# Kernel tuning notes

Measured on AMD Instinct MI355X. Metric: run time of the kernel, lower is better.

Reference implementation:

```python
import jax, jax.numpy as jnp
import numpy as np


def setup_inputs() -> dict:
    key = jax.random.key(0)
    ks = jax.random.split(key, 8)
    C = 512
    Cq = C // 8  # 64
    x = jax.random.normal(ks[0], (4, C, 64, 64), dtype=jnp.float32)
    # 1x1 conv == per-pixel linear; store weights as [out, in]
    Wq = jax.random.normal(ks[1], (Cq, C), dtype=jnp.float32) * (1.0 / np.sqrt(C))
    bq = jax.random.normal(ks[2], (Cq,), dtype=jnp.float32) * 0.01
    Wk = jax.random.normal(ks[3], (Cq, C), dtype=jnp.float32) * (1.0 / np.sqrt(C))
    bk = jax.random.normal(ks[4], (Cq,), dtype=jnp.float32) * 0.01
    Wv = jax.random.normal(ks[5], (C, C), dtype=jnp.float32) * (1.0 / np.sqrt(C))
    bv = jax.random.normal(ks[6], (C,), dtype=jnp.float32) * 0.01
    alpha = jax.random.normal(ks[7], (1,), dtype=jnp.float32)
    return {"x": x, "Wq": Wq, "bq": bq, "Wk": Wk, "bk": bk, "Wv": Wv, "bv": bv, "alpha": alpha}


def reference(x, Wq, bq, Wk, bk, Wv, bv, alpha):
    B, C, H, W = x.shape
    HW = H * W
    xf = x.reshape(B, C, HW)  # [B, C, HW]
    # 1x1 convs as channel matmuls
    q = jnp.einsum('oc,bcn->bon', Wq, xf) + bq[None, :, None]  # [B, Cq, HW]
    k = jnp.einsum('oc,bcn->bon', Wk, xf) + bk[None, :, None]  # [B, Cq, HW]
    v = jnp.einsum('oc,bcn->bon', Wv, xf) + bv[None, :, None]  # [B, C, HW]
    # attention[b, i, j] = softmax_j( q[:, i] . k[:, j] )
    scores = jnp.einsum('bci,bcj->bij', q, k)  # [B, HW, HW]
    attn = jax.nn.softmax(scores, axis=-1)
    # feat_e = v @ attn^T : out[b, c, i] = sum_j v[b, c, j] * attn[b, i, j]
    feat_e = jnp.einsum('bcj,bij->bci', v, attn).reshape(B, C, H, W)
    return alpha[0] * feat_e
```

## Files before the change

kernel.cpp:

```cpp
#include <hip/hip_runtime.h>
#include <hip/hip_fp16.h>

#define HW_N 4096
#define C_IN 512
#define C_Q  64
#define NB   4
#define M_Y  640
#define LOG2E 1.4426950408889634f

typedef __attribute__((ext_vector_type(8))) short short8;
typedef __attribute__((ext_vector_type(4))) short short4v;
typedef __attribute__((ext_vector_type(4))) float float4v;
typedef unsigned short ushort_t;

__device__ __forceinline__ ushort_t f2h(float x) {
    return __half_as_ushort(__float2half(x));
}
__device__ __forceinline__ float h2f(ushort_t h) {
    return __half2float(__ushort_as_half(h));
}
__device__ __forceinline__ void gl2lds16(const ushort_t* g, ushort_t* l) {
    __builtin_amdgcn_global_load_lds(
        (const __attribute__((address_space(1))) unsigned int*)g,
        (__attribute__((address_space(3))) unsigned int*)l, 16, 0, 0);
}

__global__ __launch_bounds__(256) void split_w(const float* __restrict__ Wq,
                                               const float* __restrict__ Wk,
                                               const float* __restrict__ Wv,
                                               ushort_t* __restrict__ Wh,
                                               ushort_t* __restrict__ Wl) {
    int idx = (blockIdx.x * 256 + threadIdx.x) * 4;
#pragma unroll
    for (int e = 0; e < 4; e++) {
        int i = idx + e;
        int m = i >> 9, k = i & 511;
        float v = (m < C_Q) ? Wq[m * C_IN + k]
                 : (m < 2 * C_Q) ? Wk[(m - C_Q) * C_IN + k]
                 : Wv[(size_t)(m - 2 * C_Q) * C_IN + k];
        ushort_t h = f2h(v);
        Wh[i] = h;
        Wl[i] = f2h(v - h2f(h));
    }
}

__global__ __launch_bounds__(256) void split_x(const float* __restrict__ x,
                                               ushort_t* __restrict__ xTh,
                                               ushort_t* __restrict__ xTl,
                                               float* __restrict__ D) {
    const size_t bz = blockIdx.z;
    x   += bz * ((size_t)C_IN * HW_N);
    xTh += bz * ((size_t)HW_N * C_IN);
    xTl += bz * ((size_t)HW_N * C_IN);
    D   += bz * HW_N;

    if (blockIdx.y == 0 && blockIdx.x < 16) D[blockIdx.x * 256 + threadIdx.x] = 0.f;

    __shared__ float tile[64][65];
    const int n0 = blockIdx.x * 64, k0 = blockIdx.y * 64;
    const int t = threadIdx.x;
#pragma unroll
    for (int it = 0; it < 4; it++) {
        int e = t + it * 256;
        int r = e >> 4, c4 = (e & 15) << 2;
        float4 v = *(const float4*)(x + (size_t)(k0 + r) * HW_N + n0 + c4);
        tile[r][c4 + 0] = v.x; tile[r][c4 + 1] = v.y;
        tile[r][c4 + 2] = v.z; tile[r][c4 + 3] = v.w;
    }
    __syncthreads();
    const int rr = t >> 2, kq = (t & 3) << 4;
    ushort_t h[16], l[16];
#pragma unroll
    for (int j = 0; j < 16; j++) {
        float v = tile[kq + j][rr];
        h[j] = f2h(v);
        l[j] = f2h(v - h2f(h[j]));
    }
    size_t o = (size_t)(n0 + rr) * C_IN + k0 + kq;
    *(uint4*)(xTh + o) = *(uint4*)h;
    *(uint4*)(xTh + o + 8) = *(uint4*)(h + 8);
    *(uint4*)(xTl + o) = *(uint4*)l;
    *(uint4*)(xTl + o + 8) = *(uint4*)(l + 8);
}

__global__ __launch_bounds__(256, 2) void ygemm(
    const ushort_t* __restrict__ Ah, const ushort_t* __restrict__ Al,
    const ushort_t* __restrict__ Bh, const ushort_t* __restrict__ Bl,
    const float* __restrict__ bq, const float* __restrict__ bk,
    const float* __restrict__ bv,
    ushort_t* __restrict__ qkTh, ushort_t* __restrict__ qkTl,
    ushort_t* __restrict__ Vh, ushort_t* __restrict__ Vl) {
    const size_t bz = blockIdx.z;
    Bh   += bz * ((size_t)HW_N * C_IN);
    Bl   += bz * ((size_t)HW_N * C_IN);
    qkTh += bz * ((size_t)HW_N * 2 * C_Q);
    qkTl += bz * ((size_t)HW_N * 2 * C_Q);
    Vh   += bz * ((size_t)C_IN * HW_N);
    Vl   += bz * ((size_t)C_IN * HW_N);

    __shared__ ushort_t sAh[2][128 * 32];
    __shared__ ushort_t sAl[2][128 * 32];
    __shared__ ushort_t sBh[2][128 * 32];
    __shared__ ushort_t sBl[2][128 * 32];

    const int tid = threadIdx.x, w = tid >> 6, lane = tid & 63;
    const int quad = lane >> 4, lr = lane & 15;
    const int m0 = blockIdx.y * 128, n0 = blockIdx.x * 128;

    const ushort_t* src;
    ushort_t* dst0;
    int rowBase;
    if (w == 0)      { src = Ah; dst0 = sAh[0]; rowBase = m0; }
    else if (w == 1) { src = Al; dst0 = sAl[0]; rowBase = m0; }
    else if (w == 2) { src = Bh; dst0 = sBh[0]; rowBase = n0; }
    else             { src = Bl; dst0 = sBl[0]; rowBase = n0; }
    const int cr = lane >> 2, uv = lane & 3;
    const int kcol = (uv ^ ((cr >> 1) & 3)) << 3;
    const ushort_t* gk = src + (size_t)(rowBase + cr) * C_IN + kcol;

    const int wm = (w & 1) * 64, wn = (w >> 1) * 64;
    const int up = (quad ^ ((lr >> 1) & 3)) << 3;

    float4v acc[4][4];
#pragma unroll
    for (int i = 0; i < 4; i++)
#pragma unroll
        for (int j = 0; j < 4; j++) acc[i][j] = (float4v){0.f, 0.f, 0.f, 0.f};

#pragma unroll
    for (int c = 0; c < 8; c++)
        gl2lds16(gk + (size_t)(c * 16) * C_IN, dst0 + c * 512);
    __syncthreads();

    const int NSTEP = C_IN / 32;
    for (int it = 0; it < NSTEP; ++it) {
        const int cur = it & 1, nxt = cur ^ 1;

        if (it + 1 < NSTEP) {
            ushort_t* db = dst0 + nxt * (128 * 32);
#pragma unroll
            for (int c = 0; c < 8; c++)
                gl2lds16(gk + (size_t)(c * 16) * C_IN + (it + 1) * 32, db + c * 512);
        }

        short8 ah[4], al[4], bh[4], bl[4];
#pragma unroll
        for (int i = 0; i < 4; i++) {
            ah[i] = *(const short8*)&sAh[cur][(wm + i * 16 + lr) * 32 + up];
            al[i] = *(const short8*)&sAl[cur][(wm + i * 16 + lr) * 32 + up];
            bh[i] = *(const short8*)&sBh[cur][(wn + i * 16 + lr) * 32 + up];
            bl[i] = *(const short8*)&sBl[cur][(wn + i * 16 + lr) * 32 + up];
        }
#pragma unroll
        for (int i = 0; i < 4; i++)
#pragma unroll
            for (int j = 0; j < 4; j++)
                acc[i][j] = __builtin_amdgcn_mfma_f32_16x16x32_f16(ah[i], bh[j], acc[i][j], 0, 0, 0);
#pragma unroll
        for (int i = 0; i < 4; i++)
#pragma unroll
            for (int j = 0; j < 4; j++)
                acc[i][j] = __builtin_amdgcn_mfma_f32_16x16x32_f16(ah[i], bl[j], acc[i][j], 0, 0, 0);
#pragma unroll
        for (int i = 0; i < 4; i++)
#pragma unroll
            for (int j = 0; j < 4; j++)
                acc[i][j] = __builtin_amdgcn_mfma_f32_16x16x32_f16(al[i], bh[j], acc[i][j], 0, 0, 0);
        __syncthreads();
    }

#pragma unroll
    for (int i = 0; i < 4; i++)
#pragma unroll
        for (int j = 0; j < 4; j++)
#pragma unroll
            for (int r = 0; r < 4; r++) {
                const int m = m0 + wm + i * 16 + quad * 4 + r;
                const int n = n0 + wn + j * 16 + lr;
                float bi = (m < C_Q) ? bq[m]
                          : (m < 2 * C_Q) ? bk[m - C_Q] : bv[m - 2 * C_Q];
                float v = acc[i][j][r] + bi;
                ushort_t h = f2h(v);
                ushort_t lo = f2h(v - h2f(h));
                if (m < 2 * C_Q) {
                    qkTh[(size_t)n * (2 * C_Q) + m] = h;
                    qkTl[(size_t)n * (2 * C_Q) + m] = lo;
                } else {
                    Vh[(size_t)(m - 2 * C_Q) * HW_N + n] = h;
                    Vl[(size_t)(m - 2 * C_Q) * HW_N + n] = lo;
                }
            }
}

__global__ __launch_bounds__(256, 2) void qkgemm(const ushort_t* __restrict__ qkTh_,
                                                 const ushort_t* __restrict__ qkTl_,
                                                 float* __restrict__ outF,
                                                 float* __restrict__ Dsum) {
    __shared__ ushort_t sAh[2][128 * 32];
    __shared__ ushort_t sAl[2][128 * 32];
    __shared__ ushort_t sBh[2][128 * 32];
    __shared__ ushort_t sBl[2][128 * 32];

    const int tid = threadIdx.x, w = tid >> 6, lane = tid & 63;
    const int quad = lane >> 4, lr = lane & 15;
    const int m0 = blockIdx.y * 128, n0 = blockIdx.x * 128;

    const ushort_t* src = ((w & 1) ? qkTl_ : qkTh_) + ((w >> 1) ? C_Q : 0);
    ushort_t* dst0 = (w == 0) ? sAh[0] : (w == 1) ? sAl[0]
                   : (w == 2) ? sBh[0] : sBl[0];
    const int rowBase = (w >> 1) ? n0 : m0;
    const int cr = lane >> 2, uv = lane & 3;
    const int kcol = (uv ^ ((cr >> 1) & 3)) << 3;
    const ushort_t* gk = src + (size_t)(rowBase + cr) * (2 * C_Q) + kcol;

    const int wm = (w & 1) * 64, wn = (w >> 1) * 64;
    const int up = (quad ^ ((lr >> 1) & 3)) << 3;

    float4v acc[4][4];
#pragma unroll
    for (int i = 0; i < 4; i++)
#pragma unroll
        for (int j = 0; j < 4; j++) acc[i][j] = (float4v){0.f, 0.f, 0.f, 0.f};

#pragma unroll
    for (int c = 0; c < 8; c++)
        gl2lds16(gk + (size_t)(c * 16) * (2 * C_Q), dst0 + c * 512);
    __syncthreads();

    const int NSTEP = C_Q / 32;
#pragma unroll
    for (int it = 0; it < NSTEP; ++it) {
        const int cur = it & 1, nxt = cur ^ 1;

        if (it + 1 < NSTEP) {
            ushort_t* db = dst0 + nxt * (128 * 32);
#pragma unroll
            for (int c = 0; c < 8; c++)
                gl2lds16(gk + (size_t)(c * 16) * (2 * C_Q) + (it + 1) * 32, db + c * 512);
        }

        short8 ah[4], al[4], bh[4], bl[4];
#pragma unroll
        for (int i = 0; i < 4; i++) {
            ah[i] = *(const short8*)&sAh[cur][(wm + i * 16 + lr) * 32 + up];
            al[i] = *(const short8*)&sAl[cur][(wm + i * 16 + lr) * 32 + up];
            bh[i] = *(const short8*)&sBh[cur][(wn + i * 16 + lr) * 32 + up];
            bl[i] = *(const short8*)&sBl[cur][(wn + i * 16 + lr) * 32 + up];
        }
#pragma unroll
        for (int i = 0; i < 4; i++)
#pragma unroll
            for (int j = 0; j < 4; j++)
                acc[i][j] = __builtin_amdgcn_mfma_f32_16x16x32_f16(ah[i], bh[j], acc[i][j], 0, 0, 0);
#pragma unroll
        for (int i = 0; i < 4; i++)
#pragma unroll
            for (int j = 0; j < 4; j++)
                acc[i][j] = __builtin_amdgcn_mfma_f32_16x16x32_f16(ah[i], bl[j], acc[i][j], 0, 0, 0);
#pragma unroll
        for (int i = 0; i < 4; i++)
#pragma unroll
            for (int j = 0; j < 4; j++)
                acc[i][j] = __builtin_amdgcn_mfma_f32_16x16x32_f16(al[i], bh[j], acc[i][j], 0, 0, 0);
        if (it + 1 < NSTEP) __syncthreads();
    }

#pragma unroll
    for (int i = 0; i < 4; i++) {
#pragma unroll
        for (int r = 0; r < 4; r++) {
            float s = 0.f;
#pragma unroll
            for (int j = 0; j < 4; j++) {
                const int m = m0 + wm + i * 16 + quad * 4 + r;
                const int n = n0 + wn + j * 16 + lr;
                outF[(size_t)m * HW_N + n] = acc[i][j][r];
                s += __expf(acc[i][j][r]);
            }
            s += __shfl_xor(s, 1);
            s += __shfl_xor(s, 2);
            s += __shfl_xor(s, 4);
            s += __shfl_xor(s, 8);
            if (lr == 0)
                atomicAdd(&Dsum[m0 + wm + i * 16 + quad * 4 + r], s);
        }
    }
}

__global__ __launch_bounds__(512, 2) void feat7(const ushort_t* __restrict__ Vh,
                                                const ushort_t* __restrict__ Vl,
                                                const float* __restrict__ S,
                                                const float* __restrict__ D,
                                                float* __restrict__ out,
                                                float* __restrict__ part,
                                                int kLen) {
    __shared__ ushort_t sVh[2][256 * 32];
    __shared__ ushort_t sVl[2][256 * 32];
    __shared__ ushort_t sP [2][256 * 32];

    const int tid = threadIdx.x, w = tid >> 6, lane = tid & 63;
    const int quad = lane >> 4, lr = lane & 15;
    const int m0 = blockIdx.y * 256, n0 = blockIdx.x * 256;
    const int k0 = blockIdx.z * kLen;

    const int crv = lane >> 2, uv = lane & 3;
    const int vcol = (uv ^ ((crv >> 1) & 3)) << 3;
    const ushort_t* vbase = (w < 4) ? Vh : Vl;
    const ushort_t* gVsrc[4];
    int sOfs[4];
#pragma unroll
    for (int c = 0; c < 4; c++) {
        const int chunk = ((w & 3) * 4 + c);
        gVsrc[c] = vbase + (size_t)(m0 + chunk * 16 + crv) * HW_N + vcol + k0;
        sOfs[c] = chunk * 512;
    }

    const int pr = tid >> 3, pu = tid & 7;
    const float* gS = S + (size_t)(n0 + pr) * HW_N + k0 + pu * 4;
    const int pdst = (((pu >> 1) ^ ((pr >> 1) & 3)) << 3) + ((pu & 1) << 2);
    float lrw[4];
#pragma unroll
    for (int c = 0; c < 4; c++) lrw[c] = -log2f(D[n0 + pr + 64 * c]);

    const int wm = (w & 3) * 64, wn = (w >> 2) * 128;

    float4 sreg[4];
    const int nIter = kLen >> 5;

    {
#pragma unroll
        for (int c = 0; c < 4; c++)
            sreg[c] = *(const float4*)(gS + (size_t)(64 * c) * HW_N);
#pragma unroll
        for (int c = 0; c < 4; c++) gl2lds16(gVsrc[c], ((w < 4) ? sVh : sVl)[0] + sOfs[c]);
#pragma unroll
        for (int c = 0; c < 4; c++) {
            ushort_t h4[4];
            h4[0] = f2h(exp2f(fmaf(sreg[c].x, LOG2E, lrw[c])));
            h4[1] = f2h(exp2f(fmaf(sreg[c].y, LOG2E, lrw[c])));
            h4[2] = f2h(exp2f(fmaf(sreg[c].z, LOG2E, lrw[c])));
            h4[3] = f2h(exp2f(fmaf(sreg[c].w, LOG2E, lrw[c])));
            *(short4v*)&sP[0][(pr + 64 * c) * 32 + pdst] = *(short4v*)h4;
        }
        if (nIter > 1) {
#pragma unroll
            for (int c = 0; c < 4; c++)
                sreg[c] = *(const float4*)(gS + (size_t)(64 * c) * HW_N + 32);
        }
    }
    __syncthreads();

    float4v acc[4][8];
#pragma unroll
    for (int i = 0; i < 4; i++)
#pragma unroll
        for (int j = 0; j < 8; j++) acc[i][j] = (float4v){0.f, 0.f, 0.f, 0.f};

    for (int it = 0; it < nIter; ++it) {
        const int kk = it << 5;
        const int cur = it & 1, nxt = cur ^ 1;

        if (it + 1 < nIter) {
            ushort_t* db = ((w < 4) ? sVh : sVl)[nxt];
#pragma unroll
            for (int c = 0; c < 4; c++) gl2lds16(gVsrc[c] + kk + 32, db + sOfs[c]);
        }

        short8 bh[8];
#pragma unroll
        for (int j = 0; j < 8; j++) {
            const int row = wn + j * 16 + lr;
            bh[j] = *(const short8*)&sP[cur][row * 32 + ((quad ^ ((lr >> 1) & 3)) << 3)];
        }

        if (it + 1 < nIter) {
#pragma unroll
            for (int c = 0; c < 4; c++) {
                ushort_t h4[4];
                h4[0] = f2h(exp2f(fmaf(sreg[c].x, LOG2E, lrw[c])));
                h4[1] = f2h(exp2f(fmaf(sreg[c].y, LOG2E, lrw[c])));
                h4[2] = f2h(exp2f(fmaf(sreg[c].z, LOG2E, lrw[c])));
                h4[3] = f2h(exp2f(fmaf(sreg[c].w, LOG2E, lrw[c])));
                *(short4v*)&sP[nxt][(pr + 64 * c) * 32 + pdst] = *(short4v*)h4;
            }
            if (it + 2 < nIter) {
#pragma unroll
                for (int c = 0; c < 4; c++)
                    sreg[c] = *(const float4*)(gS + (size_t)(64 * c) * HW_N + kk + 64);
            }
        }

#pragma unroll
        for (int i = 0; i < 4; i++) {
            const int row = wm + i * 16 + lr;
            const int up = (quad ^ ((lr >> 1) & 3)) << 3;
            short8 ah = *(const short8*)&sVh[cur][row * 32 + up];
            short8 al = *(const short8*)&sVl[cur][row * 32 + up];
#pragma unroll
            for (int j = 0; j < 8; j++)
                acc[i][j] = __builtin_amdgcn_mfma_f32_16x16x32_f16(ah, bh[j], acc[i][j], 0, 0, 0);
#pragma unroll
            for (int j = 0; j < 8; j++)
                acc[i][j] = __builtin_amdgcn_mfma_f32_16x16x32_f16(al, bh[j], acc[i][j], 0, 0, 0);
        }
        __syncthreads();
    }

    float* o = (blockIdx.z == 0) ? out
             : (part + (size_t)(blockIdx.z - 1) * ((size_t)C_IN * HW_N));
#pragma unroll
    for (int i = 0; i < 4; i++)
#pragma unroll
        for (int j = 0; j < 8; j++)
#pragma unroll
            for (int r = 0; r < 4; r++) {
                const int m = m0 + wm + i * 16 + quad * 4 + r;
                const int n = n0 + wn + j * 16 + lr;
                o[(size_t)m * HW_N + n] = acc[i][j][r];
            }
}

__global__ __launch_bounds__(256) void reduce_alphaN(float* __restrict__ out,
                                                     const float4* __restrict__ part,
                                                     size_t stride4,
                                                     const float* __restrict__ alpha,
                                                     int np) {
    const size_t i = (size_t)blockIdx.x * 256 + threadIdx.x;
    const float a = alpha[0];
    float4* out4 = (float4*)out;
    float4 s = out4[i];
    for (int p = 0; p < np; p++) {
        float4 t = part[i + (size_t)p * stride4];
        s.x += t.x; s.y += t.y; s.z += t.z; s.w += t.w;
    }
    float4 o;
    o.x = a * s.x; o.y = a * s.y; o.z = a * s.z; o.w = a * s.w;
    out4[i] = o;
}


extern "C" void kernel_launch(void* const* d_in, const int* in_sizes, int n_in,
                              void* d_out, int out_size, void* d_ws, size_t ws_size,
                              hipStream_t stream) {
    const float* x     = (const float*)d_in[0];
    const float* Wq    = (const float*)d_in[1];
    const float* bq    = (const float*)d_in[2];
    const float* Wk    = (const float*)d_in[3];
    const float* bk    = (const float*)d_in[4];
    const float* Wv    = (const float*)d_in[5];
    const float* bv    = (const float*)d_in[6];
    const float* alpha = (const float*)d_in[7];
    float* out = (float*)d_out;

    const size_t planeQK = (size_t)HW_N * 2 * C_Q;
    const size_t planeV  = (size_t)C_IN * HW_N;
    const size_t planeXT = (size_t)HW_N * C_IN;
    const size_t planeW  = (size_t)M_Y * C_IN;
    const size_t planeS  = (size_t)HW_N * HW_N;

    const size_t fusedBytes =
        (size_t)NB * HW_N * 4 + 2 * (size_t)NB * planeQK * 2 +
        2 * (size_t)NB * planeV * 2 + 2 * planeW * 2 + planeS * 4 +
        7 * planeV * 4;
    const bool fused = (ws_size >= fusedBytes);

    if (fused) {
        float* D4      = (float*)d_ws;
        ushort_t* qkTh4 = (ushort_t*)(D4 + (size_t)NB * HW_N);
        ushort_t* qkTl4 = qkTh4 + (size_t)NB * planeQK;
        ushort_t* Vh4   = qkTl4 + (size_t)NB * planeQK;
        ushort_t* Vl4   = Vh4 + (size_t)NB * planeV;
        ushort_t* Wh    = Vl4 + (size_t)NB * planeV;
        ushort_t* Wl    = Wh + planeW;
        float* scores   = (float*)(Wl + planeW);
        float* part     = scores + planeS;
        ushort_t* xTh4  = (ushort_t*)scores;
        ushort_t* xTl4  = xTh4 + (size_t)NB * planeXT;

        split_w<<<dim3(M_Y * C_IN / 4 / 256), dim3(256), 0, stream>>>(Wq, Wk, Wv, Wh, Wl);

        split_x<<<dim3(HW_N / 64, C_IN / 64, NB), dim3(256), 0, stream>>>(
            x, xTh4, xTl4, D4);
        ygemm<<<dim3(HW_N / 128, M_Y / 128, NB), dim3(256), 0, stream>>>(
            Wh, Wl, xTh4, xTl4, bq, bk, bv, qkTh4, qkTl4, Vh4, Vl4);

        for (int b = 0; b < NB; b++) {
            float* outb = out + (size_t)b * planeV;
            qkgemm<<<dim3(HW_N / 128, HW_N / 128), dim3(256), 0, stream>>>(
                qkTh4 + (size_t)b * planeQK, qkTl4 + (size_t)b * planeQK,
                scores, D4 + (size_t)b * HW_N);
            feat7<<<dim3(HW_N / 256, C_IN / 256, 8), dim3(512), 0, stream>>>(
                Vh4 + (size_t)b * planeV, Vl4 + (size_t)b * planeV,
                scores, D4 + (size_t)b * HW_N, outb, part, HW_N / 8);
            reduce_alphaN<<<dim3((C_IN * HW_N / 4) / 256), dim3(256), 0, stream>>>(
                outb, (const float4*)part, planeV / 4, alpha, 7);
        }
        return;
    }

    float* D = (float*)d_ws;
    ushort_t* qkTh = (ushort_t*)(D + HW_N);
    ushort_t* qkTl = qkTh + planeQK;
    ushort_t* Vh   = qkTl + planeQK;
    ushort_t* Vl   = Vh + planeV;
    ushort_t* Wh   = Vl + planeV;
    ushort_t* Wl   = Wh + planeW;
    float* scores  = (float*)(Wl + planeW);
    float* part    = scores + planeS;
    ushort_t* xTh  = (ushort_t*)scores;
    ushort_t* xTl  = xTh + planeXT;

    const size_t baseF = (size_t)(part - (float*)d_ws);
    const int zsplit = (ws_size >= (baseF + 7 * planeV) * sizeof(float)) ? 8 : 4;

    split_w<<<dim3(M_Y * C_IN / 4 / 256), dim3(256), 0, stream>>>(Wq, Wk, Wv, Wh, Wl);

    for (int b = 0; b < NB; b++) {
        const float* xb = x + (size_t)b * planeV;
        float* outb = out + (size_t)b * planeV;

        split_x<<<dim3(HW_N / 64, C_IN / 64, 1), dim3(256), 0, stream>>>(
            xb, xTh, xTl, D);
        ygemm<<<dim3(HW_N / 128, M_Y / 128, 1), dim3(256), 0, stream>>>(
            Wh, Wl, xTh, xTl, bq, bk, bv, qkTh, qkTl, Vh, Vl);
        qkgemm<<<dim3(HW_N / 128, HW_N / 128), dim3(256), 0, stream>>>(
            qkTh, qkTl, scores, D);
        feat7<<<dim3(HW_N / 256, C_IN / 256, zsplit), dim3(512), 0, stream>>>(
            Vh, Vl, scores, D, outb, part, HW_N / zsplit);
        reduce_alphaN<<<dim3((C_IN * HW_N / 4) / 256), dim3(256), 0, stream>>>(
            outb, (const float4*)part, planeV / 4, alpha, zsplit - 1);
    }
}
```

Before: 467.1 us.

## Enlarge ygemm tile to 256x256 with 512 threads and padded weight rows

Moves the projection GEMM from 128x128 tiles with 4 waves to 256x256 tiles with 8 waves, each wave computing a 64x128 sub-tile. The weight matrix is zero-padded from 640 to 768 rows so the M dimension divides by 256, and the rows past the real ones are skipped at store time. The goal is more operand reuse per LDS load and fewer blocks, which should cut global and LDS traffic per MFMA. The cost is about 20% wasted compute on padding rows, 128KB of LDS per block, a larger accumulator array with register pressure, and only 3x16x4 blocks in the grid.

```diff
diff --git a/kernel.cpp b/kernel.cpp
--- a/kernel.cpp
+++ b/kernel.cpp
@@ -6,6 +6,7 @@
 #define C_Q  64
 #define NB   4
 #define M_Y  640
+#define M_YP 768
 #define LOG2E 1.4426950408889634f
 
 typedef __attribute__((ext_vector_type(8))) short short8;
@@ -37,7 +38,8 @@
         int m = i >> 9, k = i & 511;
         float v = (m < C_Q) ? Wq[m * C_IN + k]
                  : (m < 2 * C_Q) ? Wk[(m - C_Q) * C_IN + k]
-                 : Wv[(size_t)(m - 2 * C_Q) * C_IN + k];
+                 : (m < M_Y) ? Wv[(size_t)(m - 2 * C_Q) * C_IN + k]
+                 : 0.f;
         ushort_t h = f2h(v);
         Wh[i] = h;
         Wl[i] = f2h(v - h2f(h));
@@ -83,7 +85,7 @@
     *(uint4*)(xTl + o + 8) = *(uint4*)(l + 8);
 }
 
-__global__ __launch_bounds__(256, 2) void ygemm(
+__global__ __launch_bounds__(512, 2) void ygemm(
     const ushort_t* __restrict__ Ah, const ushort_t* __restrict__ Al,
     const ushort_t* __restrict__ Bh, const ushort_t* __restrict__ Bl,
     const float* __restrict__ bq, const float* __restrict__ bk,
@@ -98,38 +100,40 @@
     Vh   += bz * ((size_t)C_IN * HW_N);
     Vl   += bz * ((size_t)C_IN * HW_N);
 
-    __shared__ ushort_t sAh[2][128 * 32];
-    __shared__ ushort_t sAl[2][128 * 32];
-    __shared__ ushort_t sBh[2][128 * 32];
-    __shared__ ushort_t sBl[2][128 * 32];
+    __shared__ ushort_t sAh[2][256 * 32];
+    __shared__ ushort_t sAl[2][256 * 32];
+    __shared__ ushort_t sBh[2][256 * 32];
+    __shared__ ushort_t sBl[2][256 * 32];
 
     const int tid = threadIdx.x, w = tid >> 6, lane = tid & 63;
     const int quad = lane >> 4, lr = lane & 15;
-    const int m0 = blockIdx.y * 128, n0 = blockIdx.x * 128;
-
+    const int m0 = blockIdx.y * 256, n0 = blockIdx.x * 256;
+
+    const int mat = w >> 1, half = w & 1;
     const ushort_t* src;
     ushort_t* dst0;
     int rowBase;
-    if (w == 0)      { src = Ah; dst0 = sAh[0]; rowBase = m0; }
-    else if (w == 1) { src = Al; dst0 = sAl[0]; rowBase = m0; }
-    else if (w == 2) { src = Bh; dst0 = sBh[0]; rowBase = n0; }
-    else             { src = Bl; dst0 = sBl[0]; rowBase = n0; }
+    if (mat == 0)      { src = Ah; dst0 = sAh[0]; rowBase = m0; }
+    else if (mat == 1) { src = Al; dst0 = sAl[0]; rowBase = m0; }
+    else if (mat == 2) { src = Bh; dst0 = sBh[0]; rowBase = n0; }
+    else               { src = Bl; dst0 = sBl[0]; rowBase = n0; }
     const int cr = lane >> 2, uv = lane & 3;
     const int kcol = (uv ^ ((cr >> 1) & 3)) << 3;
-    const ushort_t* gk = src + (size_t)(rowBase + cr) * C_IN + kcol;
-
-    const int wm = (w & 1) * 64, wn = (w >> 1) * 64;
+    const ushort_t* gk = src + (size_t)(rowBase + half * 128 + cr) * C_IN + kcol;
+    const int cOfs = half * 8;
+
+    const int wm = (w & 3) * 64, wn = (w >> 2) * 128;
     const int up = (quad ^ ((lr >> 1) & 3)) << 3;
 
-    float4v acc[4][4];
+    float4v acc[4][8];
 #pragma unroll
     for (int i = 0; i < 4; i++)
 #pragma unroll
-        for (int j = 0; j < 4; j++) acc[i][j] = (float4v){0.f, 0.f, 0.f, 0.f};
+        for (int j = 0; j < 8; j++) acc[i][j] = (float4v){0.f, 0.f, 0.f, 0.f};
 
 #pragma unroll
     for (int c = 0; c < 8; c++)
-        gl2lds16(gk + (size_t)(c * 16) * C_IN, dst0 + c * 512);
+        gl2lds16(gk + (size_t)(c * 16) * C_IN, dst0 + (cOfs + c) * 512);
     __syncthreads();
 
     const int NSTEP = C_IN / 32;
@@ -137,45 +141,46 @@
         const int cur = it & 1, nxt = cur ^ 1;
 
         if (it + 1 < NSTEP) {
-            ushort_t* db = dst0 + nxt * (128 * 32);
+            ushort_t* db = dst0 + nxt * (256 * 32);
 #pragma unroll
             for (int c = 0; c < 8; c++)
-                gl2lds16(gk + (size_t)(c * 16) * C_IN + (it + 1) * 32, db + c * 512);
-        }
-
-        short8 ah[4], al[4], bh[4], bl[4];
+                gl2lds16(gk + (size_t)(c * 16) * C_IN + (it + 1) * 32,
+                         db + (cOfs + c) * 512);
+        }
+
+        short8 bh[8], bl[8];
+#pragma unroll
+        for (int j = 0; j < 8; j++) {
+            const int row = wn + j * 16 + lr;
+            bh[j] = *(const short8*)&sBh[cur][row * 32 + up];
+            bl[j] = *(const short8*)&sBl[cur][row * 32 + up];
+        }
 #pragma unroll
         for (int i = 0; i < 4; i++) {
-            ah[i] = *(const short8*)&sAh[cur][(wm + i * 16 + lr) * 32 + up];
-            al[i] = *(const short8*)&sAl[cur][(wm + i * 16 + lr) * 32 + up];
-            bh[i] = *(const short8*)&sBh[cur][(wn + i * 16 + lr) * 32 + up];
-            bl[i] = *(const short8*)&sBl[cur][(wn + i * 16 + lr) * 32 + up];
-        }
-#pragma unroll
-        for (int i = 0; i < 4; i++)
-#pragma unroll
-            for (int j = 0; j < 4; j++)
-                acc[i][j] = __builtin_amdgcn_mfma_f32_16x16x32_f16(ah[i], bh[j], acc[i][j], 0, 0, 0);
-#pragma unroll
-        for (int i = 0; i < 4; i++)
-#pragma unroll
-            for (int j = 0; j < 4; j++)
-                acc[i][j] = __builtin_amdgcn_mfma_f32_16x16x32_f16(ah[i], bl[j], acc[i][j], 0, 0, 0);
-#pragma unroll
-        for (int i = 0; i < 4; i++)
-#pragma unroll
-            for (int j = 0; j < 4; j++)
-                acc[i][j] = __builtin_amdgcn_mfma_f32_16x16x32_f16(al[i], bh[j], acc[i][j], 0, 0, 0);
+            const int row = wm + i * 16 + lr;
+            short8 ah = *(const short8*)&sAh[cur][row * 32 + up];
+            short8 al = *(const short8*)&sAl[cur][row * 32 + up];
+#pragma unroll
+            for (int j = 0; j < 8; j++)
+                acc[i][j] = __builtin_amdgcn_mfma_f32_16x16x32_f16(ah, bh[j], acc[i][j], 0, 0, 0);
+#pragma unroll
+            for (int j = 0; j < 8; j++)
+                acc[i][j] = __builtin_amdgcn_mfma_f32_16x16x32_f16(ah, bl[j], acc[i][j], 0, 0, 0);
+#pragma unroll
+            for (int j = 0; j < 8; j++)
+                acc[i][j] = __builtin_amdgcn_mfma_f32_16x16x32_f16(al, bh[j], acc[i][j], 0, 0, 0);
+        }
         __syncthreads();
     }
 
 #pragma unroll
     for (int i = 0; i < 4; i++)
 #pragma unroll
-        for (int j = 0; j < 4; j++)
+        for (int j = 0; j < 8; j++)
 #pragma unroll
             for (int r = 0; r < 4; r++) {
                 const int m = m0 + wm + i * 16 + quad * 4 + r;
+                if (m >= M_Y) continue;
                 const int n = n0 + wn + j * 16 + lr;
                 float bi = (m < C_Q) ? bq[m]
                           : (m < 2 * C_Q) ? bk[m - C_Q] : bv[m - 2 * C_Q];
@@ -455,7 +460,7 @@
     const size_t planeQK = (size_t)HW_N * 2 * C_Q;
     const size_t planeV  = (size_t)C_IN * HW_N;
     const size_t planeXT = (size_t)HW_N * C_IN;
-    const size_t planeW  = (size_t)M_Y * C_IN;
+    const size_t planeW  = (size_t)M_YP * C_IN;
     const size_t planeS  = (size_t)HW_N * HW_N;
 
     const size_t fusedBytes =
@@ -477,11 +482,11 @@
         ushort_t* xTh4  = (ushort_t*)scores;
         ushort_t* xTl4  = xTh4 + (size_t)NB * planeXT;
 
-        split_w<<<dim3(M_Y * C_IN / 4 / 256), dim3(256), 0, stream>>>(Wq, Wk, Wv, Wh, Wl);
+        split_w<<<dim3(M_YP * C_IN / 4 / 256), dim3(256), 0, stream>>>(Wq, Wk, Wv, Wh, Wl);
 
         split_x<<<dim3(HW_N / 64, C_IN / 64, NB), dim3(256), 0, stream>>>(
             x, xTh4, xTl4, D4);
-        ygemm<<<dim3(HW_N / 128, M_Y / 128, NB), dim3(256), 0, stream>>>(
+        ygemm<<<dim3(HW_N / 256, M_YP / 256, NB), dim3(512), 0, stream>>>(
             Wh, Wl, xTh4, xTl4, bq, bk, bv, qkTh4, qkTl4, Vh4, Vl4);
 
         for (int b = 0; b < NB; b++) {
@@ -513,7 +518,7 @@
     const size_t baseF = (size_t)(part - (float*)d_ws);
     const int zsplit = (ws_size >= (baseF + 7 * planeV) * sizeof(float)) ? 8 : 4;
 
-    split_w<<<dim3(M_Y * C_IN / 4 / 256), dim3(256), 0, stream>>>(Wq, Wk, Wv, Wh, Wl);
+    split_w<<<dim3(M_YP * C_IN / 4 / 256), dim3(256), 0, stream>>>(Wq, Wk, Wv, Wh, Wl);
 
     for (int b = 0; b < NB; b++) {
         const float* xb = x + (size_t)b * planeV;
@@ -521,7 +526,7 @@
 
         split_x<<<dim3(HW_N / 64, C_IN / 64, 1), dim3(256), 0, stream>>>(
             xb, xTh, xTl, D);
-        ygemm<<<dim3(HW_N / 128, M_Y / 128, 1), dim3(256), 0, stream>>>(
+        ygemm<<<dim3(HW_N / 256, M_YP / 256, 1), dim3(512), 0, stream>>>(
             Wh, Wl, xTh, xTl, bq, bk, bv, qkTh, qkTl, Vh, Vl);
         qkgemm<<<dim3(HW_N / 128, HW_N / 128), dim3(256), 0, stream>>>(
             qkTh, qkTl, scores, D);
```

Result: slower. 485.9 us (+4.0%).
